# Kernel tuning notes

Measured on AMD Instinct MI355X. Metric: run time of the kernel, lower is better.

Reference implementation:

```python
import jax, jax.numpy as jnp
import numpy as np

M, N = 64, 8192
IN_DIM, HID, OUT = 6, 256, 128


def _mlp3(x, params):
    # three Linear+ReLU layers
    for W, b in params:
        x = jax.nn.relu(x @ W + b)
    return x


def setup_inputs() -> dict:
    key = jax.random.key(0)
    ks = jax.random.split(key, 16)
    def lin(k, fan_in, fan_out):
        bound = 1.0 / np.sqrt(fan_in)
        kw, kb = jax.random.split(k)
        W = jax.random.uniform(kw, (fan_in, fan_out), jnp.float32, -bound, bound)
        b = jax.random.uniform(kb, (fan_out,), jnp.float32, -bound, bound)
        return W, b
    feat = jax.random.normal(ks[0], (M, N, IN_DIM), jnp.float32)
    eW1, eb1 = lin(ks[1], IN_DIM, HID)
    eW2, eb2 = lin(ks[2], HID, HID)
    eW3, eb3 = lin(ks[3], HID, HID)
    sW1, sb1 = lin(ks[4], HID, OUT)
    sW2, sb2 = lin(ks[5], OUT, OUT)
    sW3, sb3 = lin(ks[6], OUT, OUT)
    cW, cb = lin(ks[7], IN_DIM + HID + OUT, 1)
    return {
        'feat': feat,
        'eW1': eW1, 'eb1': eb1, 'eW2': eW2, 'eb2': eb2, 'eW3': eW3, 'eb3': eb3,
        'sW1': sW1, 'sb1': sb1, 'sW2': sW2, 'sb2': sb2, 'sW3': sW3, 'sb3': sb3,
        'cW': cW, 'cb': cb,
    }


def reference(feat, eW1, eb1, eW2, eb2, eW3, eb3,
              sW1, sb1, sW2, sb2, sW3, sb3, cW, cb):
    # embed MLP over all points: [M, N, HID]
    hidden = _mlp3(feat, [(eW1, eb1), (eW2, eb2), (eW3, eb3)])
    # max-pool over points within each bbox: [M, HID]
    pooled = jnp.max(hidden, axis=1)
    # segment MLP on pooled feature: [M, OUT]
    seg = _mlp3(pooled, [(sW1, sb1), (sW2, sb2), (sW3, sb3)])
    # concat [feat, hidden, seg broadcast over points]: [M, N, 6+HID+OUT]
    seg_tiled = jnp.broadcast_to(seg[:, None, :], (feat.shape[0], feat.shape[1], seg.shape[-1]))
    concat = jnp.concatenate([feat, hidden, seg_tiled], axis=-1)
    # classifier -> score [M, N]
    score = (concat @ cW)[..., 0] + cb[0]
    # per-bbox min/max rescale to [-1, 1]
    smin = jnp.min(score, axis=1, keepdims=True)
    smax = jnp.max(score, axis=1, keepdims=True)
    score = (score - smin) / (smax - smin) * 2.0 - 1.0
    return score
```

## Files before the change

kernel.cpp:

```cpp
#include <hip/hip_runtime.h>


typedef __attribute__((ext_vector_type(8))) short short8;
typedef __attribute__((ext_vector_type(4))) float f32x4;
typedef __attribute__((ext_vector_type(4))) unsigned int u32x4;

#define THREADS 256

__device__ __forceinline__ unsigned short f2bf(float f) {
  union { float f; unsigned int u; } x; x.f = f;
  unsigned int r = x.u + 0x7fffu + ((x.u >> 16) & 1u);
  return (unsigned short)(r >> 16);
}

__device__ __forceinline__ unsigned int cvt_pk_bf16(float lo, float hi) {
  unsigned int r;
  asm("v_cvt_pk_bf16_f32 %0, %1, %2" : "=v"(r) : "v"(lo), "v"(hi));
  return r;
}

__global__ void pn_pack(const float* __restrict__ W1,
                        const float* __restrict__ W2,
                        const float* __restrict__ W3,
                        unsigned short* __restrict__ wp) {
  int e = blockIdx.x * 256 + threadIdx.x;
  const float* src; int Kreal, base, r;
  if (e < 8192)       { src = W1; Kreal = 6;   base = 0;     r = e; }
  else if (e < 73728) { src = W2; Kreal = 256; base = 8192;  r = e - 8192; }
  else                { src = W3; Kreal = 256; base = 73728; r = e - 73728; }
  int j   = r & 7;
  int col = (r >> 3) & 15;
  int hi  = (r >> 7) & 3;
  int ct  = (r >> 9) & 15;
  int s   = r >> 13;
  int k = s * 32 + hi * 8 + j;
  int c = ct * 16 + col;
  float v = (k < Kreal) ? src[k * 256 + c] : 0.0f;
  wp[base + r] = f2bf(v);
}

__device__ __forceinline__ void gemm256(const unsigned short* __restrict__ wpL,
                                        const unsigned short* hbuf,
                                        int cgrp, int l15, int hi,
                                        f32x4 (&acc)[4][4]) {
#pragma unroll
  for (int ks = 0; ks < 8; ++ks) {
    short8 afr[4], bfr[4];
#pragma unroll
    for (int cf = 0; cf < 4; ++cf) {
      int ct = cgrp * 4 + cf;
      afr[cf] = *(const short8*)(wpL + (((((ks * 16 + ct) * 4) + hi) * 16 + l15) << 3));
    }
#pragma unroll
    for (int pf = 0; pf < 4; ++pf) {
      int p = pf * 16 + l15;
      int byteoff = ((p * 256 + ks * 32 + hi * 8) * 2) ^ ((p & 7) << 4);
      bfr[pf] = *(const short8*)((const char*)hbuf + byteoff);
    }
#pragma unroll
    for (int cf = 0; cf < 4; ++cf)
#pragma unroll
      for (int pf = 0; pf < 4; ++pf)
        acc[cf][pf] = __builtin_amdgcn_mfma_f32_16x16x32_bf16(
            afr[cf], bfr[pf], acc[cf][pf], 0, 0, 0);
  }
}

__device__ __forceinline__ void acc_init(f32x4 (&acc)[4][4], const float* bv,
                                         int cgrp, int hi) {
#pragma unroll
  for (int cf = 0; cf < 4; ++cf) {
    f32x4 bi = *(const f32x4*)(bv + cgrp * 64 + cf * 16 + hi * 4);
#pragma unroll
    for (int pf = 0; pf < 4; ++pf) acc[cf][pf] = bi;
  }
}

__device__ __forceinline__ void epi_h(f32x4 (&acc)[4][4], unsigned short* dst,
                                      int cgrp, int l15, int hi) {
#pragma unroll
  for (int cf = 0; cf < 4; ++cf) {
    int c0 = cgrp * 64 + cf * 16 + hi * 4;
#pragma unroll
    for (int pf = 0; pf < 4; ++pf) {
      int p = pf * 16 + l15;
      f32x4 a = acc[cf][pf];
      unsigned int lo  = cvt_pk_bf16(fmaxf(a[0], 0.0f), fmaxf(a[1], 0.0f));
      unsigned int hi2 = cvt_pk_bf16(fmaxf(a[2], 0.0f), fmaxf(a[3], 0.0f));
      unsigned long long w = (unsigned long long)lo | ((unsigned long long)hi2 << 32);
      int byteoff = ((p * 256 + c0) * 2) ^ ((p & 7) << 4);
      *(unsigned long long*)((char*)dst + byteoff) = w;
    }
  }
}

__global__ __launch_bounds__(THREADS, 1) void pn_main(
    const float* __restrict__ feat,
    const unsigned short* __restrict__ wp,
    const float* __restrict__ b1,
    const float* __restrict__ b2,
    const float* __restrict__ b3,
    const float* __restrict__ cW,
    float* __restrict__ out) {
  __shared__ unsigned short hA[64 * 256];
  __shared__ unsigned short hF[64 * 8];
  __shared__ float biasL[3 * 256];
  __shared__ float whL[256];
  float* sPart = (float*)hF;

  const int tid  = threadIdx.x;
  const int lane = tid & 63;
  const int wave = tid >> 6;
  const int l15  = lane & 15;
  const int hi   = lane >> 4;
  const int cgrp = wave;

  const int blk = blockIdx.x;
  const int m   = blk >> 7;
  const int n0  = (blk & 127) << 6;
  const int g0  = m * 8192 + n0;

  biasL[tid]       = b1[tid & 255];
  biasL[256 + tid] = b2[tid & 255];
  biasL[512 + tid] = b3[tid & 255];
  whL[tid & 255]   = cW[6 + (tid & 255)];

  float fdot = 0.0f;
  if (tid < 64) {
    const float* fp = feat + (g0 + tid) * 6;
    float f0 = fp[0], f1 = fp[1], f2 = fp[2], f3 = fp[3], f4 = fp[4], f5 = fp[5];
    fdot = f0 * cW[0] + f1 * cW[1] + f2 * cW[2] + f3 * cW[3] + f4 * cW[4] + f5 * cW[5];
    u32x4 v;
    v[0] = cvt_pk_bf16(f0, f1);
    v[1] = cvt_pk_bf16(f2, f3);
    v[2] = cvt_pk_bf16(f4, f5);
    v[3] = 0;
    *(u32x4*)(hF + tid * 8) = v;
  }
  __syncthreads();

  f32x4 acc[4][4];
  const short8 zero8 = {0, 0, 0, 0, 0, 0, 0, 0};

  acc_init(acc, biasL + 0, cgrp, hi);
  {
    short8 afr[4], bfr[4];
#pragma unroll
    for (int cf = 0; cf < 4; ++cf) {
      int ct = cgrp * 4 + cf;
      afr[cf] = *(const short8*)(wp + (((ct * 4 + hi) * 16 + l15) << 3));
    }
#pragma unroll
    for (int pf = 0; pf < 4; ++pf) {
      int p = pf * 16 + l15;
      bfr[pf] = (hi == 0) ? *(const short8*)(hF + p * 8) : zero8;
    }
#pragma unroll
    for (int cf = 0; cf < 4; ++cf)
#pragma unroll
      for (int pf = 0; pf < 4; ++pf)
        acc[cf][pf] = __builtin_amdgcn_mfma_f32_16x16x32_bf16(
            afr[cf], bfr[pf], acc[cf][pf], 0, 0, 0);
  }
  epi_h(acc, hA, cgrp, l15, hi);
  __syncthreads();

  acc_init(acc, biasL + 256, cgrp, hi);
  gemm256(wp + 8192, hA, cgrp, l15, hi, acc);
  __syncthreads();
  epi_h(acc, hA, cgrp, l15, hi);
  __syncthreads();

  acc_init(acc, biasL + 512, cgrp, hi);
  gemm256(wp + 73728, hA, cgrp, l15, hi, acc);

  float part[4] = {0.f, 0.f, 0.f, 0.f};
#pragma unroll
  for (int cf = 0; cf < 4; ++cf) {
    int c0 = cgrp * 64 + cf * 16 + hi * 4;
#pragma unroll
    for (int r = 0; r < 4; ++r) {
      float wv = whL[c0 + r];
#pragma unroll
      for (int pf = 0; pf < 4; ++pf)
        part[pf] += fmaxf(acc[cf][pf][r], 0.0f) * wv;
    }
  }
#pragma unroll
  for (int off = 16; off < 64; off <<= 1)
#pragma unroll
    for (int pf = 0; pf < 4; ++pf)
      part[pf] += __shfl_xor(part[pf], off);
  if (hi == 0) {
#pragma unroll
    for (int pf = 0; pf < 4; ++pf)
      sPart[cgrp * 64 + pf * 16 + l15] = part[pf];
  }
  __syncthreads();

  if (tid < 64) {
    float s = sPart[tid] + sPart[64 + tid] + sPart[128 + tid] + sPart[192 + tid]
            + fdot;
    out[g0 + tid] = s;
  }
}

__global__ void pn_finalize(float* __restrict__ out) {
  __shared__ float smn[4], smx[4];
  int mrow = blockIdx.x;
  float* row = out + mrow * 8192;
  float v[32];
  float mn = 1e30f, mx = -1e30f;
#pragma unroll
  for (int i = 0; i < 32; ++i) {
    v[i] = row[threadIdx.x + i * 256];
    mn = fminf(mn, v[i]);
    mx = fmaxf(mx, v[i]);
  }
#pragma unroll
  for (int off = 1; off < 64; off <<= 1) {
    mn = fminf(mn, __shfl_xor(mn, off));
    mx = fmaxf(mx, __shfl_xor(mx, off));
  }
  int w = threadIdx.x >> 6;
  if ((threadIdx.x & 63) == 0) { smn[w] = mn; smx[w] = mx; }
  __syncthreads();
  mn = fminf(fminf(smn[0], smn[1]), fminf(smn[2], smn[3]));
  mx = fmaxf(fmaxf(smx[0], smx[1]), fmaxf(smx[2], smx[3]));
  float sc = 2.0f / (mx - mn);
#pragma unroll
  for (int i = 0; i < 32; ++i)
    row[threadIdx.x + i * 256] = (v[i] - mn) * sc - 1.0f;
}

extern "C" void kernel_launch(void* const* d_in, const int* in_sizes, int n_in,
                              void* d_out, int out_size, void* d_ws, size_t ws_size,
                              hipStream_t stream) {
  const float* feat = (const float*)d_in[0];
  const float* eW1  = (const float*)d_in[1];
  const float* eb1  = (const float*)d_in[2];
  const float* eW2  = (const float*)d_in[3];
  const float* eb2  = (const float*)d_in[4];
  const float* eW3  = (const float*)d_in[5];
  const float* eb3  = (const float*)d_in[6];
  const float* cW   = (const float*)d_in[13];
  float* out = (float*)d_out;
  unsigned short* wpack = (unsigned short*)d_ws;

  pn_pack<<<544, 256, 0, stream>>>(eW1, eW2, eW3, wpack);
  pn_main<<<8192, THREADS, 0, stream>>>(feat, wpack, eb1, eb2, eb3, cW, out);
  pn_finalize<<<64, 256, 0, stream>>>(out);
}
```

Before: 151.2 us.

## Pipeline layers 2 and 3 across wave groups in a persistent kernel with register-resident weights

```diff
diff --git a/kernel.cpp b/kernel.cpp
--- a/kernel.cpp
+++ b/kernel.cpp
@@ -5,7 +5,8 @@
 typedef __attribute__((ext_vector_type(4))) float f32x4;
 typedef __attribute__((ext_vector_type(4))) unsigned int u32x4;
 
-#define THREADS 256
+#define THREADS 512
+#define NTILES 32
 
 __device__ __forceinline__ unsigned short f2bf(float f) {
   union { float f; unsigned int u; } x; x.f = f;
@@ -39,18 +40,23 @@
   wp[base + r] = f2bf(v);
 }
 
-__device__ __forceinline__ void gemm256(const unsigned short* __restrict__ wpL,
-                                        const unsigned short* hbuf,
-                                        int cgrp, int l15, int hi,
-                                        f32x4 (&acc)[4][4]) {
+__device__ __forceinline__ void acc_init(f32x4 (&acc)[4][4], const float* bv,
+                                         int cgrp, int hi) {
+#pragma unroll
+  for (int cf = 0; cf < 4; ++cf) {
+    f32x4 bi = *(const f32x4*)(bv + cgrp * 64 + cf * 16 + hi * 4);
+#pragma unroll
+    for (int pf = 0; pf < 4; ++pf) acc[cf][pf] = bi;
+  }
+}
+
+__device__ __forceinline__ void gemm256r(const short8 (&wA)[8][4],
+                                         const unsigned short* hbuf,
+                                         int l15, int hi,
+                                         f32x4 (&acc)[4][4]) {
 #pragma unroll
   for (int ks = 0; ks < 8; ++ks) {
-    short8 afr[4], bfr[4];
-#pragma unroll
-    for (int cf = 0; cf < 4; ++cf) {
-      int ct = cgrp * 4 + cf;
-      afr[cf] = *(const short8*)(wpL + (((((ks * 16 + ct) * 4) + hi) * 16 + l15) << 3));
-    }
+    short8 bfr[4];
 #pragma unroll
     for (int pf = 0; pf < 4; ++pf) {
       int p = pf * 16 + l15;
@@ -62,17 +68,7 @@
 #pragma unroll
       for (int pf = 0; pf < 4; ++pf)
         acc[cf][pf] = __builtin_amdgcn_mfma_f32_16x16x32_bf16(
-            afr[cf], bfr[pf], acc[cf][pf], 0, 0, 0);
-  }
-}
-
-__device__ __forceinline__ void acc_init(f32x4 (&acc)[4][4], const float* bv,
-                                         int cgrp, int hi) {
-#pragma unroll
-  for (int cf = 0; cf < 4; ++cf) {
-    f32x4 bi = *(const f32x4*)(bv + cgrp * 64 + cf * 16 + hi * 4);
-#pragma unroll
-    for (int pf = 0; pf < 4; ++pf) acc[cf][pf] = bi;
+            wA[ks][cf], bfr[pf], acc[cf][pf], 0, 0, 0);
   }
 }
 
@@ -94,7 +90,7 @@
   }
 }
 
-__global__ __launch_bounds__(THREADS, 1) void pn_main(
+__global__ __launch_bounds__(THREADS, 2) void pn_pipe(
     const float* __restrict__ feat,
     const unsigned short* __restrict__ wp,
     const float* __restrict__ b1,
@@ -102,106 +98,123 @@
     const float* __restrict__ b3,
     const float* __restrict__ cW,
     float* __restrict__ out) {
-  __shared__ unsigned short hA[64 * 256];
+  __shared__ unsigned short h1[64 * 256];
+  __shared__ unsigned short h2[2][64 * 256];
   __shared__ unsigned short hF[64 * 8];
   __shared__ float biasL[3 * 256];
   __shared__ float whL[256];
-  float* sPart = (float*)hF;
+  __shared__ float fdA[4][64];
+  __shared__ float sPart[4][64];
 
   const int tid  = threadIdx.x;
   const int lane = tid & 63;
   const int wave = tid >> 6;
   const int l15  = lane & 15;
   const int hi   = lane >> 4;
-  const int cgrp = wave;
-
-  const int blk = blockIdx.x;
-  const int m   = blk >> 7;
-  const int n0  = (blk & 127) << 6;
-  const int g0  = m * 8192 + n0;
-
-  biasL[tid]       = b1[tid & 255];
-  biasL[256 + tid] = b2[tid & 255];
-  biasL[512 + tid] = b3[tid & 255];
-  whL[tid & 255]   = cW[6 + (tid & 255)];
-
-  float fdot = 0.0f;
-  if (tid < 64) {
-    const float* fp = feat + (g0 + tid) * 6;
-    float f0 = fp[0], f1 = fp[1], f2 = fp[2], f3 = fp[3], f4 = fp[4], f5 = fp[5];
-    fdot = f0 * cW[0] + f1 * cW[1] + f2 * cW[2] + f3 * cW[3] + f4 * cW[4] + f5 * cW[5];
-    u32x4 v;
-    v[0] = cvt_pk_bf16(f0, f1);
-    v[1] = cvt_pk_bf16(f2, f3);
-    v[2] = cvt_pk_bf16(f4, f5);
-    v[3] = 0;
-    *(u32x4*)(hF + tid * 8) = v;
-  }
+  const bool isA = wave < 4;
+  const int cgrp = wave & 3;
+
+  if (tid < 256) {
+    biasL[tid]       = b1[tid];
+    biasL[256 + tid] = b2[tid];
+    biasL[512 + tid] = b3[tid];
+    whL[tid]         = cW[6 + tid];
+  }
+  const float c0 = cW[0], c1 = cW[1], c2 = cW[2], c3 = cW[3], c4 = cW[4], c5 = cW[5];
+
+  short8 wA[8][4];
+  {
+    const unsigned short* wb = wp + (isA ? 8192 : 73728);
+#pragma unroll
+    for (int ks = 0; ks < 8; ++ks)
+#pragma unroll
+      for (int cf = 0; cf < 4; ++cf)
+        wA[ks][cf] = *(const short8*)(wb + (((((ks * 16 + (cgrp * 4 + cf)) * 4) + hi) * 16 + l15) << 3));
+  }
+  short8 w1r[4];
+#pragma unroll
+  for (int cf = 0; cf < 4; ++cf)
+    w1r[cf] = *(const short8*)(wp + ((((cgrp * 4 + cf) * 4 + hi) * 16 + l15) << 3));
+
+  const int tbase = blockIdx.x * NTILES;
+  const short8 zero8 = {0, 0, 0, 0, 0, 0, 0, 0};
+  f32x4 acc[4][4];
+
   __syncthreads();
 
-  f32x4 acc[4][4];
-  const short8 zero8 = {0, 0, 0, 0, 0, 0, 0, 0};
-
-  acc_init(acc, biasL + 0, cgrp, hi);
-  {
-    short8 afr[4], bfr[4];
-#pragma unroll
-    for (int cf = 0; cf < 4; ++cf) {
-      int ct = cgrp * 4 + cf;
-      afr[cf] = *(const short8*)(wp + (((ct * 4 + hi) * 16 + l15) << 3));
-    }
-#pragma unroll
-    for (int pf = 0; pf < 4; ++pf) {
-      int p = pf * 16 + l15;
-      bfr[pf] = (hi == 0) ? *(const short8*)(hF + p * 8) : zero8;
-    }
-#pragma unroll
-    for (int cf = 0; cf < 4; ++cf)
-#pragma unroll
-      for (int pf = 0; pf < 4; ++pf)
-        acc[cf][pf] = __builtin_amdgcn_mfma_f32_16x16x32_bf16(
-            afr[cf], bfr[pf], acc[cf][pf], 0, 0, 0);
-  }
-  epi_h(acc, hA, cgrp, l15, hi);
-  __syncthreads();
-
-  acc_init(acc, biasL + 256, cgrp, hi);
-  gemm256(wp + 8192, hA, cgrp, l15, hi, acc);
-  __syncthreads();
-  epi_h(acc, hA, cgrp, l15, hi);
-  __syncthreads();
-
-  acc_init(acc, biasL + 512, cgrp, hi);
-  gemm256(wp + 73728, hA, cgrp, l15, hi, acc);
-
-  float part[4] = {0.f, 0.f, 0.f, 0.f};
-#pragma unroll
-  for (int cf = 0; cf < 4; ++cf) {
-    int c0 = cgrp * 64 + cf * 16 + hi * 4;
-#pragma unroll
-    for (int r = 0; r < 4; ++r) {
-      float wv = whL[c0 + r];
-#pragma unroll
-      for (int pf = 0; pf < 4; ++pf)
-        part[pf] += fmaxf(acc[cf][pf][r], 0.0f) * wv;
-    }
-  }
-#pragma unroll
-  for (int off = 16; off < 64; off <<= 1)
-#pragma unroll
-    for (int pf = 0; pf < 4; ++pf)
-      part[pf] += __shfl_xor(part[pf], off);
-  if (hi == 0) {
-#pragma unroll
-    for (int pf = 0; pf < 4; ++pf)
-      sPart[cgrp * 64 + pf * 16 + l15] = part[pf];
-  }
-  __syncthreads();
-
-  if (tid < 64) {
-    float s = sPart[tid] + sPart[64 + tid] + sPart[128 + tid] + sPart[192 + tid]
-            + fdot;
-    out[g0 + tid] = s;
+#pragma unroll 1
+  for (int t = 0; t <= NTILES + 1; ++t) {
+    if (isA) {
+      if (t < NTILES && tid < 64) {
+        int g  = tbase + t;
+        int g0 = ((g >> 7) << 13) + ((g & 127) << 6);
+        const float* fp = feat + (size_t)(g0 + tid) * 6;
+        float f0 = fp[0], f1 = fp[1], f2 = fp[2], f3 = fp[3], f4 = fp[4], f5 = fp[5];
+        fdA[t & 3][tid] = f0 * c0 + f1 * c1 + f2 * c2 + f3 * c3 + f4 * c4 + f5 * c5;
+        u32x4 v;
+        v[0] = cvt_pk_bf16(f0, f1);
+        v[1] = cvt_pk_bf16(f2, f3);
+        v[2] = cvt_pk_bf16(f4, f5);
+        v[3] = 0;
+        *(u32x4*)(hF + tid * 8) = v;
+      }
+    } else if (wave == 4 && t >= 2) {
+      int g  = tbase + (t - 2);
+      int g0 = ((g >> 7) << 13) + ((g & 127) << 6);
+      float s = sPart[0][lane] + sPart[1][lane] + sPart[2][lane] + sPart[3][lane]
+              + fdA[(t - 2) & 3][lane];
+      out[g0 + lane] = s;
+    }
+    __syncthreads();
+
+    if (isA && t < NTILES) {
+      acc_init(acc, biasL, cgrp, hi);
+#pragma unroll
+      for (int pf = 0; pf < 4; ++pf) {
+        int p = pf * 16 + l15;
+        short8 b = (hi == 0) ? *(const short8*)(hF + p * 8) : zero8;
+#pragma unroll
+        for (int cf = 0; cf < 4; ++cf)
+          acc[cf][pf] = __builtin_amdgcn_mfma_f32_16x16x32_bf16(
+              w1r[cf], b, acc[cf][pf], 0, 0, 0);
+      }
+      epi_h(acc, h1, cgrp, l15, hi);
+    }
+    __syncthreads();
+
+    if (isA) {
+      if (t < NTILES) {
+        acc_init(acc, biasL + 256, cgrp, hi);
+        gemm256r(wA, h1, l15, hi, acc);
+        epi_h(acc, h2[t & 1], cgrp, l15, hi);
+      }
+    } else if (t >= 1 && t <= NTILES) {
+      acc_init(acc, biasL + 512, cgrp, hi);
+      gemm256r(wA, h2[(t - 1) & 1], l15, hi, acc);
+      float part[4] = {0.f, 0.f, 0.f, 0.f};
+#pragma unroll
+      for (int cf = 0; cf < 4; ++cf) {
+        int c0c = cgrp * 64 + cf * 16 + hi * 4;
+#pragma unroll
+        for (int r = 0; r < 4; ++r) {
+          float wv = whL[c0c + r];
+#pragma unroll
+          for (int pf = 0; pf < 4; ++pf)
+            part[pf] += fmaxf(acc[cf][pf][r], 0.0f) * wv;
+        }
+      }
+#pragma unroll
+      for (int off = 16; off < 64; off <<= 1)
+#pragma unroll
+        for (int pf = 0; pf < 4; ++pf)
+          part[pf] += __shfl_xor(part[pf], off);
+      if (hi == 0) {
+#pragma unroll
+        for (int pf = 0; pf < 4; ++pf)
+          sPart[cgrp][pf * 16 + l15] = part[pf];
+      }
+    }
+    __syncthreads();
   }
 }
 
@@ -248,6 +261,6 @@
   unsigned short* wpack = (unsigned short*)d_ws;
 
   pn_pack<<<544, 256, 0, stream>>>(eW1, eW2, eW3, wpack);
-  pn_main<<<8192, THREADS, 0, stream>>>(feat, wpack, eb1, eb2, eb3, cW, out);
+  pn_pipe<<<256, THREADS, 0, stream>>>(feat, wpack, eb1, eb2, eb3, cW, out);
   pn_finalize<<<64, 256, 0, stream>>>(out);
 }
```

Result: slower. 363.1 us (+140.2%).

## Double-buffer layer weights into LDS via async global_load_lds pipeline

Applied to the files above, without the earlier changes.

```diff
diff --git a/kernel.cpp b/kernel.cpp
--- a/kernel.cpp
+++ b/kernel.cpp
@@ -6,6 +6,9 @@
 typedef __attribute__((ext_vector_type(4))) unsigned int u32x4;
 
 #define THREADS 256
+
+#define LDS_AS(p) ((__attribute__((address_space(3))) unsigned int*)(p))
+#define GLB_AS(p) ((const __attribute__((address_space(1))) unsigned int*)(p))
 
 __device__ __forceinline__ unsigned short f2bf(float f) {
   union { float f; unsigned int u; } x; x.f = f;
@@ -39,30 +42,15 @@
   wp[base + r] = f2bf(v);
 }
 
-__device__ __forceinline__ void gemm256(const unsigned short* __restrict__ wpL,
-                                        const unsigned short* hbuf,
-                                        int cgrp, int l15, int hi,
-                                        f32x4 (&acc)[4][4]) {
-#pragma unroll
-  for (int ks = 0; ks < 8; ++ks) {
-    short8 afr[4], bfr[4];
-#pragma unroll
-    for (int cf = 0; cf < 4; ++cf) {
-      int ct = cgrp * 4 + cf;
-      afr[cf] = *(const short8*)(wpL + (((((ks * 16 + ct) * 4) + hi) * 16 + l15) << 3));
-    }
-#pragma unroll
-    for (int pf = 0; pf < 4; ++pf) {
-      int p = pf * 16 + l15;
-      int byteoff = ((p * 256 + ks * 32 + hi * 8) * 2) ^ ((p & 7) << 4);
-      bfr[pf] = *(const short8*)((const char*)hbuf + byteoff);
-    }
-#pragma unroll
-    for (int cf = 0; cf < 4; ++cf)
-#pragma unroll
-      for (int pf = 0; pf < 4; ++pf)
-        acc[cf][pf] = __builtin_amdgcn_mfma_f32_16x16x32_bf16(
-            afr[cf], bfr[pf], acc[cf][pf], 0, 0, 0);
+
+__device__ __forceinline__ void stage16k(const unsigned short* __restrict__ gsrc,
+                                         unsigned short* lbase,
+                                         int wave, int lane) {
+#pragma unroll
+  for (int r = 0; r < 4; ++r) {
+    const unsigned short* g = gsrc + (((r * 4 + wave) * 64 + lane) << 3);
+    unsigned short* l = lbase + (((r * 4 + wave) * 64) << 3);
+    __builtin_amdgcn_global_load_lds(GLB_AS(g), LDS_AS(l), 16, 0, 0);
   }
 }
 
@@ -103,6 +91,7 @@
     const float* __restrict__ cW,
     float* __restrict__ out) {
   __shared__ unsigned short hA[64 * 256];
+  __shared__ unsigned short wst[2][8192];
   __shared__ unsigned short hF[64 * 8];
   __shared__ float biasL[3 * 256];
   __shared__ float whL[256];
@@ -119,6 +108,8 @@
   const int m   = blk >> 7;
   const int n0  = (blk & 127) << 6;
   const int g0  = m * 8192 + n0;
+
+  stage16k(wp + 8192, wst[0], wave, lane);
 
   biasL[tid]       = b1[tid & 255];
   biasL[256 + tid] = b2[tid & 255];
@@ -137,23 +128,51 @@
     v[3] = 0;
     *(u32x4*)(hF + tid * 8) = v;
   }
+
+  short8 w1r[4];
+#pragma unroll
+  for (int cf = 0; cf < 4; ++cf)
+    w1r[cf] = *(const short8*)(wp + ((((cgrp * 4 + cf) * 4 + hi) * 16 + l15) << 3));
+
   __syncthreads();
 
   f32x4 acc[4][4];
   const short8 zero8 = {0, 0, 0, 0, 0, 0, 0, 0};
 
   acc_init(acc, biasL + 0, cgrp, hi);
-  {
+#pragma unroll
+  for (int pf = 0; pf < 4; ++pf) {
+    int p = pf * 16 + l15;
+    short8 b = (hi == 0) ? *(const short8*)(hF + p * 8) : zero8;
+#pragma unroll
+    for (int cf = 0; cf < 4; ++cf)
+      acc[cf][pf] = __builtin_amdgcn_mfma_f32_16x16x32_bf16(
+          w1r[cf], b, acc[cf][pf], 0, 0, 0);
+  }
+  epi_h(acc, hA, cgrp, l15, hi);
+  acc_init(acc, biasL + 256, cgrp, hi);
+
+  asm volatile("s_waitcnt vmcnt(0)");
+  __syncthreads();
+
+#pragma unroll 1
+  for (int t = 0; t < 16; ++t) {
+    if (t + 1 < 16) {
+      const unsigned short* src = wp +
+          ((t + 1 < 8) ? (8192 + (t + 1) * 8192) : (73728 + (t - 7) * 8192));
+      stage16k(src, wst[(t + 1) & 1], wave, lane);
+    }
+    const unsigned short* wt = wst[t & 1];
     short8 afr[4], bfr[4];
 #pragma unroll
-    for (int cf = 0; cf < 4; ++cf) {
-      int ct = cgrp * 4 + cf;
-      afr[cf] = *(const short8*)(wp + (((ct * 4 + hi) * 16 + l15) << 3));
-    }
+    for (int cf = 0; cf < 4; ++cf)
+      afr[cf] = *(const short8*)(wt + ((((cgrp * 4 + cf) * 4 + hi) * 16 + l15) << 3));
+    int ksl = t & 7;
 #pragma unroll
     for (int pf = 0; pf < 4; ++pf) {
       int p = pf * 16 + l15;
-      bfr[pf] = (hi == 0) ? *(const short8*)(hF + p * 8) : zero8;
+      int byteoff = ((p * 256 + ksl * 32 + hi * 8) * 2) ^ ((p & 7) << 4);
+      bfr[pf] = *(const short8*)((const char*)hA + byteoff);
     }
 #pragma unroll
     for (int cf = 0; cf < 4; ++cf)
@@ -161,18 +180,15 @@
       for (int pf = 0; pf < 4; ++pf)
         acc[cf][pf] = __builtin_amdgcn_mfma_f32_16x16x32_bf16(
             afr[cf], bfr[pf], acc[cf][pf], 0, 0, 0);
-  }
-  epi_h(acc, hA, cgrp, l15, hi);
-  __syncthreads();
-
-  acc_init(acc, biasL + 256, cgrp, hi);
-  gemm256(wp + 8192, hA, cgrp, l15, hi, acc);
-  __syncthreads();
-  epi_h(acc, hA, cgrp, l15, hi);
-  __syncthreads();
-
-  acc_init(acc, biasL + 512, cgrp, hi);
-  gemm256(wp + 73728, hA, cgrp, l15, hi, acc);
+
+    if (t == 7) {
+      __syncthreads();
+      epi_h(acc, hA, cgrp, l15, hi);
+      acc_init(acc, biasL + 512, cgrp, hi);
+    }
+    asm volatile("s_waitcnt vmcnt(0)");
+    __syncthreads();
+  }
 
   float part[4] = {0.f, 0.f, 0.f, 0.f};
 #pragma unroll
```

After: 206.4 us. 1.37x slower.
